# Kernel optimization log

Hardware: AMD Instinct MI355X
Metric: run time of the kernel (lower is better)

Reference implementation:

```python
import jax, jax.numpy as jnp
import numpy as np

TGT, SRC, BATCH, HID, ATT = 64, 64, 32, 512, 512

def setup_inputs() -> dict:
    key = jax.random.key(0)
    k1, k2, k3, k4 = jax.random.split(key, 4)
    h_t = jax.random.normal(k1, (TGT, BATCH, HID), dtype=jnp.float32)
    src_encodings = jax.random.normal(k2, (SRC, BATCH, HID), dtype=jnp.float32)
    # Wa: Linear(2*HID -> ATT, bias=False); stored as (in, out) for jnp.
    Wa = jax.random.normal(k3, (2 * HID, ATT), dtype=jnp.float32) * (1.0 / np.sqrt(2 * HID))
    # Va: Linear(ATT -> 1, bias=False)
    Va = jax.random.normal(k4, (ATT,), dtype=jnp.float32) * (1.0 / np.sqrt(ATT))
    return {"h_t": h_t, "src_encodings": src_encodings, "Wa": Wa, "Va": Va}

def reference(h_t, src_encodings, Wa, Va):
    # Wa([h_t, src]) = h_t @ Wa_h + src @ Wa_s (exact by linearity of concat-matmul)
    Wa_h, Wa_s = Wa[:HID], Wa[HID:]                 # (H, A) each
    h_part = jnp.einsum('tbh,ha->tba', h_t, Wa_h)   # (T, B, A)
    s_part = jnp.einsum('sbh,ha->sba', src_encodings, Wa_s)  # (S, B, A)
    # scores[s, t, b] = Va . tanh(h_part[t,b] + s_part[s,b])
    hidden = jnp.tanh(h_part[None, :, :, :] + s_part[:, None, :, :])  # (S, T, B, A)
    scores = jnp.einsum('stba,a->stb', hidden, Va)  # (S, T, B)
    attn = jax.nn.softmax(scores, axis=0)           # softmax over src dim
    # context[t,b,:] = sum_s attn[s,t,b] * src[s,b,:]
    context = jnp.einsum('stb,sbh->tbh', attn, src_encodings)  # (T, B, H)
    return context
```

## Files before the change

### kernel.cpp

```cpp
#include <hip/hip_runtime.h>
#include <hip/hip_bf16.h>

#define TGT   64
#define SRCN  64
#define BATCH 32
#define HID   512
#define ATT   512

typedef __bf16 bf16_t;
typedef __bf16 bf16x8 __attribute__((ext_vector_type(8)));
typedef float  f32x4  __attribute__((ext_vector_type(4)));

__device__ __forceinline__ float fast_exp2(float x) {
#if __has_builtin(__builtin_amdgcn_exp2f)
  return __builtin_amdgcn_exp2f(x);
#else
  return exp2f(x);
#endif
}

__device__ __forceinline__ float fast_rcp(float x) {
#if __has_builtin(__builtin_amdgcn_rcpf)
  return __builtin_amdgcn_rcpf(x);
#else
  return 1.0f / x;
#endif
}

__device__ __forceinline__ float tanh_fast(float x) {
  float t = fast_exp2(x * 2.8853900817779268f);
  return 1.0f - 2.0f * fast_rcp(t + 1.0f);
}

#define MFMA(a, b, c) __builtin_amdgcn_mfma_f32_16x16x32_bf16((a), (b), (c), 0, 0, 0)

__global__ __launch_bounds__(256) void proj_gemm(
    const float* __restrict__ h_t, const float* __restrict__ srcp,
    const float* __restrict__ Wa, float* __restrict__ ws)
{
  const int z = blockIdx.z;
  const float* __restrict__ A = z ? srcp : h_t;
  const float* __restrict__ B = Wa + z * (HID * ATT);
  float* __restrict__ C = ws + (size_t)z * (TGT * BATCH * ATT);

  const int mbase = blockIdx.x * 64;
  const int nbase = blockIdx.y * 64;

  __shared__ bf16_t Ahi[64][40];
  __shared__ bf16_t Alo[64][40];
  __shared__ bf16_t Bhi[64][40];
  __shared__ bf16_t Blo[64][40];

  const int tid  = threadIdx.x;
  const int lane = tid & 63;
  const int wv   = tid >> 6;
  const int wm   = (wv & 1) * 32;
  const int wn   = (wv >> 1) * 32;
  const int l15  = lane & 15;
  const int qd   = lane >> 4;

  f32x4 acc00 = {0.f, 0.f, 0.f, 0.f};
  f32x4 acc01 = acc00, acc10 = acc00, acc11 = acc00;

  const int am = tid >> 2;
  const int ak = (tid & 3) * 8;
  const int bk = tid >> 3;
  const int bn = (tid & 7) * 8;

  const float* Aptr = A + (size_t)(mbase + am) * HID + ak;
  const float* Bptr = B + (size_t)bk * ATT + nbase + bn;

  for (int kb = 0; kb < HID; kb += 32) {
    if (kb) __syncthreads();

    float4 a0 = *(const float4*)(Aptr + kb);
    float4 a1 = *(const float4*)(Aptr + kb + 4);
    float av[8] = {a0.x, a0.y, a0.z, a0.w, a1.x, a1.y, a1.z, a1.w};
    bf16x8 ah, al;
#pragma unroll
    for (int j = 0; j < 8; ++j) {
      bf16_t hi = (bf16_t)av[j];
      ah[j] = hi;
      al[j] = (bf16_t)(av[j] - (float)hi);
    }
    *(bf16x8*)&Ahi[am][ak] = ah;
    *(bf16x8*)&Alo[am][ak] = al;

    float4 b0 = *(const float4*)(Bptr + (size_t)kb * ATT);
    float4 b1 = *(const float4*)(Bptr + (size_t)kb * ATT + 4);
    float bvv[8] = {b0.x, b0.y, b0.z, b0.w, b1.x, b1.y, b1.z, b1.w};
#pragma unroll
    for (int j = 0; j < 8; ++j) {
      bf16_t hi = (bf16_t)bvv[j];
      Bhi[bn + j][bk] = hi;
      Blo[bn + j][bk] = (bf16_t)(bvv[j] - (float)hi);
    }
    __syncthreads();

    bf16x8 ah0 = *(const bf16x8*)&Ahi[wm + l15][qd * 8];
    bf16x8 ah1 = *(const bf16x8*)&Ahi[wm + 16 + l15][qd * 8];
    bf16x8 al0 = *(const bf16x8*)&Alo[wm + l15][qd * 8];
    bf16x8 al1 = *(const bf16x8*)&Alo[wm + 16 + l15][qd * 8];
    bf16x8 bh0 = *(const bf16x8*)&Bhi[wn + l15][qd * 8];
    bf16x8 bh1 = *(const bf16x8*)&Bhi[wn + 16 + l15][qd * 8];
    bf16x8 bl0 = *(const bf16x8*)&Blo[wn + l15][qd * 8];
    bf16x8 bl1 = *(const bf16x8*)&Blo[wn + 16 + l15][qd * 8];

    acc00 = MFMA(ah0, bh0, acc00);
    acc01 = MFMA(ah0, bh1, acc01);
    acc10 = MFMA(ah1, bh0, acc10);
    acc11 = MFMA(ah1, bh1, acc11);
    acc00 = MFMA(ah0, bl0, acc00);
    acc01 = MFMA(ah0, bl1, acc01);
    acc10 = MFMA(ah1, bl0, acc10);
    acc11 = MFMA(ah1, bl1, acc11);
    acc00 = MFMA(al0, bh0, acc00);
    acc01 = MFMA(al0, bh1, acc01);
    acc10 = MFMA(al1, bh0, acc10);
    acc11 = MFMA(al1, bh1, acc11);
  }

#pragma unroll
  for (int r = 0; r < 4; ++r) {
    int row0 = mbase + wm + qd * 4 + r;
    int row1 = row0 + 16;
    int col0 = nbase + wn + l15;
    C[(size_t)row0 * ATT + col0]      = acc00[r];
    C[(size_t)row0 * ATT + col0 + 16] = acc01[r];
    C[(size_t)row1 * ATT + col0]      = acc10[r];
    C[(size_t)row1 * ATT + col0 + 16] = acc11[r];
  }
}

__global__ __launch_bounds__(256) void attn_fused(
    const float* __restrict__ ws, const float* __restrict__ srcp,
    const float* __restrict__ Va, float* __restrict__ out)
{
  const float* __restrict__ h_part = ws;
  const float* __restrict__ s_part = ws + (size_t)TGT * BATCH * ATT;

  const int t0   = blockIdx.x * 4;
  const int b    = blockIdx.y;
  const int tid  = threadIdx.x;
  const int lane = tid & 63;
  const int wv   = tid >> 6;

  __shared__ float scoreLds[4][64];
  __shared__ float attnLds[4][64];

  const int abase = lane * 8;
  float va[8], H[4][8];
  *(float4*)&va[0] = *(const float4*)(Va + abase);
  *(float4*)&va[4] = *(const float4*)(Va + abase + 4);
#pragma unroll
  for (int t = 0; t < 4; ++t) {
    const float* hp = h_part + ((size_t)(t0 + t) * BATCH + b) * ATT + abase;
    *(float4*)&H[t][0] = *(const float4*)hp;
    *(float4*)&H[t][4] = *(const float4*)(hp + 4);
  }

#pragma unroll 2
  for (int i = 0; i < 16; ++i) {
    const int s = wv * 16 + i;
    const float* sp = s_part + ((size_t)s * BATCH + b) * ATT + abase;
    float4 s0 = *(const float4*)sp;
    float4 s1 = *(const float4*)(sp + 4);
    float sv[8] = {s0.x, s0.y, s0.z, s0.w, s1.x, s1.y, s1.z, s1.w};
    float p0 = 0.f, p1 = 0.f, p2 = 0.f, p3 = 0.f;
#pragma unroll
    for (int j = 0; j < 8; ++j) {
      float xv = sv[j];
      float vj = va[j];
      p0 = fmaf(tanh_fast(xv + H[0][j]), vj, p0);
      p1 = fmaf(tanh_fast(xv + H[1][j]), vj, p1);
      p2 = fmaf(tanh_fast(xv + H[2][j]), vj, p2);
      p3 = fmaf(tanh_fast(xv + H[3][j]), vj, p3);
    }
#pragma unroll
    for (int off = 32; off; off >>= 1) {
      p0 += __shfl_xor(p0, off);
      p1 += __shfl_xor(p1, off);
      p2 += __shfl_xor(p2, off);
      p3 += __shfl_xor(p3, off);
    }
    if (lane == 0) {
      scoreLds[0][s] = p0;
      scoreLds[1][s] = p1;
      scoreLds[2][s] = p2;
      scoreLds[3][s] = p3;
    }
  }
  __syncthreads();

  {
    float sc = scoreLds[wv][lane];
    float m = sc;
#pragma unroll
    for (int off = 32; off; off >>= 1) m = fmaxf(m, __shfl_xor(m, off));
    float e = fast_exp2((sc - m) * 1.4426950408889634f);
    float ssum = e;
#pragma unroll
    for (int off = 32; off; off >>= 1) ssum += __shfl_xor(ssum, off);
    attnLds[wv][lane] = e * fast_rcp(ssum);
  }
  __syncthreads();

  const int hp2 = tid * 2;
  float2 c0 = {0.f, 0.f}, c1 = c0, c2 = c0, c3 = c0;
  const float* sb = srcp + (size_t)b * HID + hp2;
#pragma unroll 4
  for (int s = 0; s < SRCN; ++s) {
    float2 sv = *(const float2*)(sb + (size_t)s * BATCH * HID);
    float a0 = attnLds[0][s], a1 = attnLds[1][s];
    float a2 = attnLds[2][s], a3 = attnLds[3][s];
    c0.x = fmaf(a0, sv.x, c0.x); c0.y = fmaf(a0, sv.y, c0.y);
    c1.x = fmaf(a1, sv.x, c1.x); c1.y = fmaf(a1, sv.y, c1.y);
    c2.x = fmaf(a2, sv.x, c2.x); c2.y = fmaf(a2, sv.y, c2.y);
    c3.x = fmaf(a3, sv.x, c3.x); c3.y = fmaf(a3, sv.y, c3.y);
  }
  *(float2*)(out + ((size_t)(t0 + 0) * BATCH + b) * HID + hp2) = c0;
  *(float2*)(out + ((size_t)(t0 + 1) * BATCH + b) * HID + hp2) = c1;
  *(float2*)(out + ((size_t)(t0 + 2) * BATCH + b) * HID + hp2) = c2;
  *(float2*)(out + ((size_t)(t0 + 3) * BATCH + b) * HID + hp2) = c3;
}

extern "C" void kernel_launch(void* const* d_in, const int* in_sizes, int n_in,
                              void* d_out, int out_size, void* d_ws, size_t ws_size,
                              hipStream_t stream) {
  const float* h_t = (const float*)d_in[0];
  const float* src = (const float*)d_in[1];
  const float* Wa  = (const float*)d_in[2];
  const float* Va  = (const float*)d_in[3];
  float* out = (float*)d_out;
  float* ws  = (float*)d_ws;

  proj_gemm<<<dim3(32, 8, 2), 256, 0, stream>>>(h_t, src, Wa, ws);
  attn_fused<<<dim3(16, 32), 256, 0, stream>>>(ws, src, Va, out);
}
```

Measured before the change: 118.8 us.

## Retile projection GEMM to 64x128 and fold tanh algebra into attention scores

The projection GEMM now uses 512-thread blocks with 64x128 output tiles and a K step of 64. The B tile is loaded in packed bf16 pairs so fewer barrier-separated iterations are needed. In the attention kernel the tanh scale is folded into h_part and s_part up front, and the score is computed as sum(Va) - 2*sum(Va/(exp+1)). That drops per-element operations from the inner loop. The exp2/rcp helpers change from the AMDGCN builtins to exp2f and __frcp_rn, which may compile to slower, more precise sequences and cancel the savings.

```diff
diff --git a/kernel.cpp b/kernel.cpp
--- a/kernel.cpp
+++ b/kernel.cpp
@@ -6,50 +6,35 @@
 #define BATCH 32
 #define HID   512
 #define ATT   512
+#define MROWS (TGT * BATCH)
 
 typedef __bf16 bf16_t;
 typedef __bf16 bf16x8 __attribute__((ext_vector_type(8)));
 typedef float  f32x4  __attribute__((ext_vector_type(4)));
 
-__device__ __forceinline__ float fast_exp2(float x) {
-#if __has_builtin(__builtin_amdgcn_exp2f)
-  return __builtin_amdgcn_exp2f(x);
-#else
-  return exp2f(x);
-#endif
-}
-
-__device__ __forceinline__ float fast_rcp(float x) {
-#if __has_builtin(__builtin_amdgcn_rcpf)
-  return __builtin_amdgcn_rcpf(x);
-#else
-  return 1.0f / x;
-#endif
-}
-
-__device__ __forceinline__ float tanh_fast(float x) {
-  float t = fast_exp2(x * 2.8853900817779268f);
-  return 1.0f - 2.0f * fast_rcp(t + 1.0f);
-}
+__device__ __forceinline__ float fast_exp2(float x) { return exp2f(x); }
+__device__ __forceinline__ float fast_rcp(float x)  { return __frcp_rn(x) ; }
 
 #define MFMA(a, b, c) __builtin_amdgcn_mfma_f32_16x16x32_bf16((a), (b), (c), 0, 0, 0)
 
-__global__ __launch_bounds__(256) void proj_gemm(
+__device__ __forceinline__ unsigned short bfbits(float f) {
+  bf16_t h = (bf16_t)f;
+  return __builtin_bit_cast(unsigned short, h);
+}
+
+__global__ __launch_bounds__(512) void proj_gemm(
     const float* __restrict__ h_t, const float* __restrict__ srcp,
-    const float* __restrict__ Wa, float* __restrict__ ws)
+    const float* __restrict__ Wa, float* __restrict__ C)
 {
   const int z = blockIdx.z;
   const float* __restrict__ A = z ? srcp : h_t;
-  const float* __restrict__ B = Wa + z * (HID * ATT);
-  float* __restrict__ C = ws + (size_t)z * (TGT * BATCH * ATT);
-
   const int mbase = blockIdx.x * 64;
-  const int nbase = blockIdx.y * 64;
-
-  __shared__ bf16_t Ahi[64][40];
-  __shared__ bf16_t Alo[64][40];
-  __shared__ bf16_t Bhi[64][40];
-  __shared__ bf16_t Blo[64][40];
+  const int nbase = blockIdx.y * 128;
+
+  __shared__ bf16_t Ah[64][72];
+  __shared__ bf16_t Al[64][72];
+  __shared__ bf16_t Bh[128][72];
+  __shared__ bf16_t Bl[128][72];
 
   const int tid  = threadIdx.x;
   const int lane = tid & 63;
@@ -59,76 +44,89 @@
   const int l15  = lane & 15;
   const int qd   = lane >> 4;
 
+  const int arow = tid >> 3;
+  const int akc  = (tid & 7) * 8;
+  const int kp = tid >> 4;
+  const int nb = tid & 15;
+
+  const float* Aptr = A + (size_t)(mbase + arow) * HID + akc;
+  const float* Bptr = Wa + (size_t)(z * HID + 2 * kp) * ATT + nbase + nb;
+
   f32x4 acc00 = {0.f, 0.f, 0.f, 0.f};
   f32x4 acc01 = acc00, acc10 = acc00, acc11 = acc00;
 
-  const int am = tid >> 2;
-  const int ak = (tid & 3) * 8;
-  const int bk = tid >> 3;
-  const int bn = (tid & 7) * 8;
-
-  const float* Aptr = A + (size_t)(mbase + am) * HID + ak;
-  const float* Bptr = B + (size_t)bk * ATT + nbase + bn;
-
-  for (int kb = 0; kb < HID; kb += 32) {
+  for (int kb = 0; kb < HID; kb += 64) {
     if (kb) __syncthreads();
 
-    float4 a0 = *(const float4*)(Aptr + kb);
-    float4 a1 = *(const float4*)(Aptr + kb + 4);
-    float av[8] = {a0.x, a0.y, a0.z, a0.w, a1.x, a1.y, a1.z, a1.w};
-    bf16x8 ah, al;
-#pragma unroll
-    for (int j = 0; j < 8; ++j) {
-      bf16_t hi = (bf16_t)av[j];
-      ah[j] = hi;
-      al[j] = (bf16_t)(av[j] - (float)hi);
-    }
-    *(bf16x8*)&Ahi[am][ak] = ah;
-    *(bf16x8*)&Alo[am][ak] = al;
-
-    float4 b0 = *(const float4*)(Bptr + (size_t)kb * ATT);
-    float4 b1 = *(const float4*)(Bptr + (size_t)kb * ATT + 4);
-    float bvv[8] = {b0.x, b0.y, b0.z, b0.w, b1.x, b1.y, b1.z, b1.w};
-#pragma unroll
-    for (int j = 0; j < 8; ++j) {
-      bf16_t hi = (bf16_t)bvv[j];
-      Bhi[bn + j][bk] = hi;
-      Blo[bn + j][bk] = (bf16_t)(bvv[j] - (float)hi);
+    {
+      float4 a0 = *(const float4*)(Aptr + kb);
+      float4 a1 = *(const float4*)(Aptr + kb + 4);
+      float av[8] = {a0.x, a0.y, a0.z, a0.w, a1.x, a1.y, a1.z, a1.w};
+      bf16x8 hi, lo;
+#pragma unroll
+      for (int j = 0; j < 8; ++j) {
+        bf16_t h = (bf16_t)av[j];
+        hi[j] = h;
+        lo[j] = (bf16_t)(av[j] - (float)h);
+      }
+      *(bf16x8*)&Ah[arow][akc] = hi;
+      *(bf16x8*)&Al[arow][akc] = lo;
+    }
+
+    {
+      const float* bp = Bptr + (size_t)kb * ATT;
+#pragma unroll
+      for (int j = 0; j < 8; ++j) {
+        float w0 = bp[16 * j];
+        float w1 = bp[ATT + 16 * j];
+        bf16_t h0 = (bf16_t)w0, h1 = (bf16_t)w1;
+        float lo0 = w0 - (float)h0, lo1 = w1 - (float)h1;
+        unsigned int uh = (unsigned int)__builtin_bit_cast(unsigned short, h0) |
+                          ((unsigned int)__builtin_bit_cast(unsigned short, h1) << 16);
+        unsigned int ul = (unsigned int)bfbits(lo0) | ((unsigned int)bfbits(lo1) << 16);
+        *(unsigned int*)&Bh[nb + 16 * j][2 * kp] = uh;
+        *(unsigned int*)&Bl[nb + 16 * j][2 * kp] = ul;
+      }
     }
     __syncthreads();
 
-    bf16x8 ah0 = *(const bf16x8*)&Ahi[wm + l15][qd * 8];
-    bf16x8 ah1 = *(const bf16x8*)&Ahi[wm + 16 + l15][qd * 8];
-    bf16x8 al0 = *(const bf16x8*)&Alo[wm + l15][qd * 8];
-    bf16x8 al1 = *(const bf16x8*)&Alo[wm + 16 + l15][qd * 8];
-    bf16x8 bh0 = *(const bf16x8*)&Bhi[wn + l15][qd * 8];
-    bf16x8 bh1 = *(const bf16x8*)&Bhi[wn + 16 + l15][qd * 8];
-    bf16x8 bl0 = *(const bf16x8*)&Blo[wn + l15][qd * 8];
-    bf16x8 bl1 = *(const bf16x8*)&Blo[wn + 16 + l15][qd * 8];
-
-    acc00 = MFMA(ah0, bh0, acc00);
-    acc01 = MFMA(ah0, bh1, acc01);
-    acc10 = MFMA(ah1, bh0, acc10);
-    acc11 = MFMA(ah1, bh1, acc11);
-    acc00 = MFMA(ah0, bl0, acc00);
-    acc01 = MFMA(ah0, bl1, acc01);
-    acc10 = MFMA(ah1, bl0, acc10);
-    acc11 = MFMA(ah1, bl1, acc11);
-    acc00 = MFMA(al0, bh0, acc00);
-    acc01 = MFMA(al0, bh1, acc01);
-    acc10 = MFMA(al1, bh0, acc10);
-    acc11 = MFMA(al1, bh1, acc11);
-  }
-
+#pragma unroll
+    for (int h = 0; h < 2; ++h) {
+      const int kh = h * 32 + qd * 8;
+      bf16x8 ah0 = *(const bf16x8*)&Ah[wm + l15][kh];
+      bf16x8 ah1 = *(const bf16x8*)&Ah[wm + 16 + l15][kh];
+      bf16x8 al0 = *(const bf16x8*)&Al[wm + l15][kh];
+      bf16x8 al1 = *(const bf16x8*)&Al[wm + 16 + l15][kh];
+      bf16x8 bh0 = *(const bf16x8*)&Bh[wn + l15][kh];
+      bf16x8 bh1 = *(const bf16x8*)&Bh[wn + 16 + l15][kh];
+      bf16x8 bl0 = *(const bf16x8*)&Bl[wn + l15][kh];
+      bf16x8 bl1 = *(const bf16x8*)&Bl[wn + 16 + l15][kh];
+
+      acc00 = MFMA(ah0, bh0, acc00);
+      acc01 = MFMA(ah0, bh1, acc01);
+      acc10 = MFMA(ah1, bh0, acc10);
+      acc11 = MFMA(ah1, bh1, acc11);
+      acc00 = MFMA(al0, bh0, acc00);
+      acc01 = MFMA(al0, bh1, acc01);
+      acc10 = MFMA(al1, bh0, acc10);
+      acc11 = MFMA(al1, bh1, acc11);
+      acc00 = MFMA(ah0, bl0, acc00);
+      acc01 = MFMA(ah0, bl1, acc01);
+      acc10 = MFMA(ah1, bl0, acc10);
+      acc11 = MFMA(ah1, bl1, acc11);
+    }
+  }
+
+  float* Cz = C + (size_t)z * (MROWS * ATT);
 #pragma unroll
   for (int r = 0; r < 4; ++r) {
     int row0 = mbase + wm + qd * 4 + r;
     int row1 = row0 + 16;
     int col0 = nbase + wn + l15;
-    C[(size_t)row0 * ATT + col0]      = acc00[r];
-    C[(size_t)row0 * ATT + col0 + 16] = acc01[r];
-    C[(size_t)row1 * ATT + col0]      = acc10[r];
-    C[(size_t)row1 * ATT + col0 + 16] = acc11[r];
+    Cz[(size_t)row0 * ATT + col0]      = acc00[r];
+    Cz[(size_t)row0 * ATT + col0 + 16] = acc01[r];
+    Cz[(size_t)row1 * ATT + col0]      = acc10[r];
+    Cz[(size_t)row1 * ATT + col0 + 16] = acc11[r];
   }
 }
 
@@ -138,6 +136,7 @@
 {
   const float* __restrict__ h_part = ws;
   const float* __restrict__ s_part = ws + (size_t)TGT * BATCH * ATT;
+  const float SC = 2.8853900817779268f;
 
   const int t0   = blockIdx.x * 4;
   const int b    = blockIdx.y;
@@ -152,11 +151,20 @@
   float va[8], H[4][8];
   *(float4*)&va[0] = *(const float4*)(Va + abase);
   *(float4*)&va[4] = *(const float4*)(Va + abase + 4);
+
+  float vsum = 0.f;
+#pragma unroll
+  for (int j = 0; j < 8; ++j) vsum += va[j];
+#pragma unroll
+  for (int off = 32; off; off >>= 1) vsum += __shfl_xor(vsum, off);
+
 #pragma unroll
   for (int t = 0; t < 4; ++t) {
     const float* hp = h_part + ((size_t)(t0 + t) * BATCH + b) * ATT + abase;
-    *(float4*)&H[t][0] = *(const float4*)hp;
-    *(float4*)&H[t][4] = *(const float4*)(hp + 4);
+    float4 h0 = *(const float4*)hp;
+    float4 h1 = *(const float4*)(hp + 4);
+    H[t][0] = h0.x * SC; H[t][1] = h0.y * SC; H[t][2] = h0.z * SC; H[t][3] = h0.w * SC;
+    H[t][4] = h1.x * SC; H[t][5] = h1.y * SC; H[t][6] = h1.z * SC; H[t][7] = h1.w * SC;
   }
 
 #pragma unroll 2
@@ -165,29 +173,30 @@
     const float* sp = s_part + ((size_t)s * BATCH + b) * ATT + abase;
     float4 s0 = *(const float4*)sp;
     float4 s1 = *(const float4*)(sp + 4);
-    float sv[8] = {s0.x, s0.y, s0.z, s0.w, s1.x, s1.y, s1.z, s1.w};
-    float p0 = 0.f, p1 = 0.f, p2 = 0.f, p3 = 0.f;
+    float sv[8] = {s0.x * SC, s0.y * SC, s0.z * SC, s0.w * SC,
+                   s1.x * SC, s1.y * SC, s1.z * SC, s1.w * SC};
+    float q0 = 0.f, q1 = 0.f, q2 = 0.f, q3 = 0.f;
 #pragma unroll
     for (int j = 0; j < 8; ++j) {
       float xv = sv[j];
       float vj = va[j];
-      p0 = fmaf(tanh_fast(xv + H[0][j]), vj, p0);
-      p1 = fmaf(tanh_fast(xv + H[1][j]), vj, p1);
-      p2 = fmaf(tanh_fast(xv + H[2][j]), vj, p2);
-      p3 = fmaf(tanh_fast(xv + H[3][j]), vj, p3);
+      q0 = fmaf(vj, fast_rcp(fast_exp2(xv + H[0][j]) + 1.0f), q0);
+      q1 = fmaf(vj, fast_rcp(fast_exp2(xv + H[1][j]) + 1.0f), q1);
+      q2 = fmaf(vj, fast_rcp(fast_exp2(xv + H[2][j]) + 1.0f), q2);
+      q3 = fmaf(vj, fast_rcp(fast_exp2(xv + H[3][j]) + 1.0f), q3);
     }
 #pragma unroll
     for (int off = 32; off; off >>= 1) {
-      p0 += __shfl_xor(p0, off);
-      p1 += __shfl_xor(p1, off);
-      p2 += __shfl_xor(p2, off);
-      p3 += __shfl_xor(p3, off);
+      q0 += __shfl_xor(q0, off);
+      q1 += __shfl_xor(q1, off);
+      q2 += __shfl_xor(q2, off);
+      q3 += __shfl_xor(q3, off);
     }
     if (lane == 0) {
-      scoreLds[0][s] = p0;
-      scoreLds[1][s] = p1;
-      scoreLds[2][s] = p2;
-      scoreLds[3][s] = p3;
+      scoreLds[0][s] = vsum - 2.0f * q0;
+      scoreLds[1][s] = vsum - 2.0f * q1;
+      scoreLds[2][s] = vsum - 2.0f * q2;
+      scoreLds[3][s] = vsum - 2.0f * q3;
     }
   }
   __syncthreads();
@@ -232,8 +241,8 @@
   const float* Wa  = (const float*)d_in[2];
   const float* Va  = (const float*)d_in[3];
   float* out = (float*)d_out;
-  float* ws  = (float*)d_ws;
-
-  proj_gemm<<<dim3(32, 8, 2), 256, 0, stream>>>(h_t, src, Wa, ws);
-  attn_fused<<<dim3(16, 32), 256, 0, stream>>>(ws, src, Va, out);
-}
+  float* C   = (float*)d_ws;
+
+  proj_gemm<<<dim3(32, 4, 2), 512, 0, stream>>>(h_t, src, Wa, C);
+  attn_fused<<<dim3(16, 32), 256, 0, stream>>>(C, src, Va, out);
+}
```

Result: slower. 133.3 us (+12.2%).
